# Kernel tuning notes

Hardware: AMD Instinct MI355X
Metric: run time of the kernel (lower is better)

The kernel has to match this reference:

```python
import jax, jax.numpy as jnp
import numpy as np

B, N, E, H, NE = 8, 512, 512, 8, 16384
DH = E // H
SCALE = DH ** -0.5
EPS = 1e-5


def _layernorm(x, g, b):
    mu = jnp.mean(x, axis=-1, keepdims=True)
    var = jnp.var(x, axis=-1, keepdims=True)
    return (x - mu) / jnp.sqrt(var + EPS) * g + b


def setup_inputs() -> dict:
    key = jax.random.key(0)
    ks = jax.random.split(key, 24)
    s = 0.02
    return {
        "x": jax.random.normal(ks[0], (B, N, E), jnp.float32),
        "edge_attr": jax.random.normal(ks[1], (NE, E), jnp.float32),
        "Wq": jax.random.normal(ks[2], (E, E), jnp.float32) * s,
        "bq": jnp.zeros((E,), jnp.float32),
        "Wk": jax.random.normal(ks[3], (E, E), jnp.float32) * s,
        "bk": jnp.zeros((E,), jnp.float32),
        "Wv": jax.random.normal(ks[4], (E, E), jnp.float32) * s,
        "bv": jnp.zeros((E,), jnp.float32),
        "Wo": jax.random.normal(ks[5], (E, E), jnp.float32) * s,
        "bo": jnp.zeros((E,), jnp.float32),
        "dist_table": jax.random.normal(ks[6], (100, H), jnp.float32),
        "We": jax.random.normal(ks[7], (H, E), jnp.float32) * s,
        "be": jnp.zeros((H,), jnp.float32),
        "W1": jax.random.normal(ks[8], (4 * E, E), jnp.float32) * s,
        "b1": jnp.zeros((4 * E,), jnp.float32),
        "W2": jax.random.normal(ks[9], (E, 4 * E), jnp.float32) * s,
        "b2": jnp.zeros((E,), jnp.float32),
        "g1": jnp.ones((E,), jnp.float32),
        "beta1": jnp.zeros((E,), jnp.float32),
        "g2": jnp.ones((E,), jnp.float32),
        "beta2": jnp.zeros((E,), jnp.float32),
        "edge_index": jax.random.randint(ks[10], (2, NE), 0, N, jnp.int64),
        "distance_matrix": jax.random.randint(ks[11], (B, N, N), 0, 100, jnp.int32),
    }


def reference(x, edge_attr, Wq, bq, Wk, bk, Wv, bv, Wo, bo, dist_table, We, be,
              W1, b1, W2, b2, g1, beta1, g2, beta2, edge_index, distance_matrix):
    residual = x
    h = _layernorm(x, g1, beta1)
    # projections -> [B, H, N, DH]
    def proj(W, b):
        return (h @ W.T + b).reshape(B, N, H, DH).transpose(0, 2, 1, 3)
    q, k, v = proj(Wq, bq), proj(Wk, bk), proj(Wv, bv)
    attn = jnp.einsum('bhnd,bhmd->bhnm', q, k) * SCALE
    # distance-encoding gather: [B,N,N] -> [B,N,N,H] -> [B,H,N,N]
    d_idx = jnp.clip(distance_matrix, 0, 99)
    attn = attn + dist_table[d_idx].transpose(0, 3, 1, 2)
    # per-edge scatter-add bias (duplicates accumulate, matching sequential loop)
    edge_enc = (edge_attr @ We.T + be).T  # [H, NE]
    src, tgt = edge_index[0], edge_index[1]
    edge_bias = jnp.zeros((H, N, N), attn.dtype).at[:, src, tgt].add(edge_enc)
    attn = attn + edge_bias[None]
    attn = jax.nn.softmax(attn, axis=-1)
    out = jnp.einsum('bhnm,bhmd->bhnd', attn, v)
    out = out.transpose(0, 2, 1, 3).reshape(B, N, E)
    out = out @ Wo.T + bo
    x1 = residual + out
    h2 = _layernorm(x1, g2, beta2)
    ffn = jax.nn.gelu(h2 @ W1.T + b1, approximate=False) @ W2.T + b2
    return x1 + ffn
```

## Files before the change

kernel.cpp:

```cpp
#include <hip/hip_runtime.h>
#include <cstdint>
#include <cstddef>

#define B_  8
#define N_  512
#define E_  512
#define H_  8
#define DH_ 64
#define NE_ 16384
#define QT  64

using u16   = unsigned short;
using bf16x8 = __attribute__((ext_vector_type(8))) __bf16;
using u16x8  = __attribute__((ext_vector_type(8))) unsigned short;
using f32x4  = __attribute__((ext_vector_type(4))) float;

__device__ __forceinline__ u16 f2b(float f) {
  unsigned u = __builtin_bit_cast(unsigned, f);
  u += 0x7fffu + ((u >> 16) & 1u);
  return (u16)(u >> 16);
}

__device__ __forceinline__ bf16x8 ld_frag(const u16* p) {
  return __builtin_bit_cast(bf16x8, *(const u16x8*)p);
}

__device__ __forceinline__ void gld_lds16(const u16* g, u16* l) {
  __builtin_amdgcn_global_load_lds(
      (const __attribute__((address_space(1))) unsigned*)(g),
      (__attribute__((address_space(3))) unsigned*)(l), 16, 0, 0);
}

__device__ __forceinline__ void gemm_core_128x128(
    const u16* __restrict__ At, int lda,
    const u16* __restrict__ Bt, int ldb, int K,
    u16* ldsA, u16* ldsB, f32x4 (&acc)[4][4]) {
  const int tid  = threadIdx.x;
  const int wid  = tid >> 6, lane = tid & 63;
  const int wr   = wid >> 1, wc = wid & 1;
  const int qd   = lane >> 4, r = lane & 15;
  const int mrow = tid >> 2, k0 = (tid & 3) * 8;
  const int wbase = wid << 9;
  for (int kt = 0; kt < K; kt += 32) {
    __syncthreads();
    gld_lds16(&At[(size_t)mrow*lda + kt + k0],        ldsA + wbase);
    gld_lds16(&At[(size_t)(mrow+64)*lda + kt + k0],   ldsA + 64*32 + wbase);
    gld_lds16(&Bt[(size_t)mrow*ldb + kt + k0],        ldsB + wbase);
    gld_lds16(&Bt[(size_t)(mrow+64)*ldb + kt + k0],   ldsB + 64*32 + wbase);
    __syncthreads();
    bf16x8 af[4], bfv[4];
#pragma unroll
    for (int i = 0; i < 4; ++i) af[i] = ld_frag(&ldsA[(wr*64 + i*16 + r)*32 + qd*8]);
#pragma unroll
    for (int j = 0; j < 4; ++j) bfv[j] = ld_frag(&ldsB[(wc*64 + j*16 + r)*32 + qd*8]);
#pragma unroll
    for (int i = 0; i < 4; ++i)
#pragma unroll
      for (int j = 0; j < 4; ++j)
        acc[i][j] = __builtin_amdgcn_mfma_f32_16x16x32_bf16(af[i], bfv[j], acc[i][j], 0, 0, 0);
  }
}

template <int EPI>
__global__ __launch_bounds__(256) void gemm_epi(
    const u16* __restrict__ A, const u16* __restrict__ W,
    const float* __restrict__ bias, const float* __restrict__ res,
    float* __restrict__ outf, u16* __restrict__ outb, int Kd, int Nd) {
  __shared__ u16 ldsA[128*32];
  __shared__ u16 ldsB[128*32];
  const int bx = blockIdx.x, by = blockIdx.y;
  f32x4 acc[4][4] = {};
  gemm_core_128x128(A + (size_t)bx*128*Kd, Kd, W + (size_t)by*128*Kd, Kd, Kd,
                    ldsA, ldsB, acc);
  const int tid = threadIdx.x, wid = tid>>6, lane = tid&63;
  const int wr = wid>>1, wc = wid&1, qd = lane>>4, r = lane&15;
#pragma unroll
  for (int i = 0; i < 4; ++i) {
#pragma unroll
    for (int j = 0; j < 4; ++j) {
      const int grow = bx*128 + wr*64 + i*16 + qd*4;
      const int gcol = by*128 + wc*64 + j*16 + r;
      const float bb = bias[gcol];
#pragma unroll
      for (int rg = 0; rg < 4; ++rg) {
        float v = acc[i][j][rg] + bb;
        const size_t idx = (size_t)(grow + rg)*Nd + gcol;
        if constexpr (EPI == 0) {
          outb[idx] = f2b(v);
        } else if constexpr (EPI == 1) {
          outf[idx] = v + res[idx];
        } else {
          v = 0.5f * v * (1.0f + erff(v * 0.70710678118f));
          outb[idx] = f2b(v);
        }
      }
    }
  }
}

__global__ __launch_bounds__(256) void gemm_splitk_k(
    const u16* __restrict__ A, const u16* __restrict__ W,
    float* __restrict__ part, int Kd, int Nd, int Ks) {
  __shared__ u16 ldsA[128*32];
  __shared__ u16 ldsB[128*32];
  const int bx = blockIdx.x, by = blockIdx.y, s = blockIdx.z;
  f32x4 acc[4][4] = {};
  gemm_core_128x128(A + (size_t)bx*128*Kd + (size_t)s*Ks, Kd,
                    W + (size_t)by*128*Kd + (size_t)s*Ks, Kd, Ks,
                    ldsA, ldsB, acc);
  const int tid = threadIdx.x, wid = tid>>6, lane = tid&63;
  const int wr = wid>>1, wc = wid&1, qd = lane>>4, r = lane&15;
  float* po = part + (size_t)s*(B_*N_)*Nd;
#pragma unroll
  for (int i = 0; i < 4; ++i) {
#pragma unroll
    for (int j = 0; j < 4; ++j) {
      const int grow = bx*128 + wr*64 + i*16 + qd*4;
      const int gcol = by*128 + wc*64 + j*16 + r;
#pragma unroll
      for (int rg = 0; rg < 4; ++rg)
        po[(size_t)(grow + rg)*Nd + gcol] = acc[i][j][rg];
    }
  }
}

template <int S>
__global__ __launch_bounds__(256) void splitk_reduce_k(
    const float* __restrict__ part, const float* __restrict__ bias,
    const float* __restrict__ res, float* __restrict__ out) {
  const size_t base = ((size_t)blockIdx.x*256 + threadIdx.x) * 4;
  float4 v = *(const float4*)&res[base];
  const int col = (int)(base & (E_-1));
  const float4 bb = *(const float4*)&bias[col];
  v.x += bb.x; v.y += bb.y; v.z += bb.z; v.w += bb.w;
#pragma unroll
  for (int s = 0; s < S; ++s) {
    const float4 p = *(const float4*)&part[(size_t)s*(B_*N_*E_) + base];
    v.x += p.x; v.y += p.y; v.z += p.z; v.w += p.w;
  }
  *(float4*)&out[base] = v;
}

__device__ __forceinline__ void ln_store(
    float v0, float v1, const float* __restrict__ g,
    const float* __restrict__ be, u16* __restrict__ outb, int row, int t) {
  float s = v0 + v1, ss = v0*v0 + v1*v1;
  for (int o = 32; o; o >>= 1) { s += __shfl_down(s, o); ss += __shfl_down(ss, o); }
  __shared__ float rs[4], rss[4];
  const int wid = t>>6, lane = t&63;
  if (!lane) { rs[wid] = s; rss[wid] = ss; }
  __syncthreads();
  s  = rs[0]+rs[1]+rs[2]+rs[3];
  ss = rss[0]+rss[1]+rss[2]+rss[3];
  const float mu   = s * (1.0f/E_);
  const float var  = ss * (1.0f/E_) - mu*mu;
  const float rstd = rsqrtf(var + 1e-5f);
  outb[(size_t)row*E_ + t]       = f2b((v0-mu)*rstd*g[t] + be[t]);
  outb[(size_t)row*E_ + t + 256] = f2b((v1-mu)*rstd*g[t+256] + be[t+256]);
}

__global__ __launch_bounds__(256) void splitk_reduce_ln_k(
    const float* __restrict__ part, const float* __restrict__ bias,
    const float* __restrict__ res, float* __restrict__ x1,
    const float* __restrict__ g, const float* __restrict__ be,
    u16* __restrict__ h2b) {
  const int row = blockIdx.x, t = threadIdx.x;
  const size_t base = (size_t)row*E_;
  float v0 = res[base + t]       + bias[t];
  float v1 = res[base + t + 256] + bias[t + 256];
#pragma unroll
  for (int s = 0; s < 2; ++s) {
    v0 += part[(size_t)s*(B_*N_*E_) + base + t];
    v1 += part[(size_t)s*(B_*N_*E_) + base + t + 256];
  }
  x1[base + t] = v0; x1[base + t + 256] = v1;
  ln_store(v0, v1, g, be, h2b, row, t);
}

__global__ __launch_bounds__(256) void qkv_gemm_k(
    const u16* __restrict__ A,
    const u16* __restrict__ Wqb, const u16* __restrict__ Wkb, const u16* __restrict__ Wvb,
    const float* __restrict__ bq, const float* __restrict__ bk, const float* __restrict__ bv,
    u16* __restrict__ qo, u16* __restrict__ ko, u16* __restrict__ vo) {
  __shared__ u16 ldsA[128*32];
  __shared__ u16 ldsB[128*32];
  const int bx = blockIdx.x, by = blockIdx.y, z = blockIdx.z;
  const u16*   W    = z == 0 ? Wqb : (z == 1 ? Wkb : Wvb);
  const float* bias = z == 0 ? bq  : (z == 1 ? bk  : bv);
  u16*         outb = z == 0 ? qo  : (z == 1 ? ko  : vo);
  f32x4 acc[4][4] = {};
  gemm_core_128x128(A + (size_t)bx*128*E_, E_, W + (size_t)by*128*E_, E_, E_,
                    ldsA, ldsB, acc);
  const int tid = threadIdx.x, wid = tid>>6, lane = tid&63;
  const int wr = wid>>1, wc = wid&1, qd = lane>>4, r = lane&15;
#pragma unroll
  for (int i = 0; i < 4; ++i) {
#pragma unroll
    for (int j = 0; j < 4; ++j) {
      const int grow = bx*128 + wr*64 + i*16 + qd*4;
      const int gcol = by*128 + wc*64 + j*16 + r;
      const float bb = bias[gcol];
#pragma unroll
      for (int rg = 0; rg < 4; ++rg)
        outb[(size_t)(grow + rg)*E_ + gcol] = f2b(acc[i][j][rg] + bb);
    }
  }
}

__global__ __launch_bounds__(256) void flash_attn_k(
    const u16* __restrict__ qm, const u16* __restrict__ km, const u16* __restrict__ vm,
    const float* __restrict__ dtab, const int* __restrict__ Dm,
    const float* __restrict__ ebias, u16* __restrict__ outb) {
  __shared__ u16 sK[2*128*32];
  __shared__ u16 sP[64*136];
  __shared__ u16 sVt[64*136];
  __shared__ float sDt[104];
  __shared__ float sMax[2][QT], sSum[2][QT], sM[QT], sL[QT], sAlpha[QT];

  const int bx = blockIdx.x;
  const int bz = blockIdx.y; const int b = bz>>3, h = bz&7;
  const int n0 = bx*QT;
  const int tid = threadIdx.x, wid = tid>>6, lane = tid&63;
  const int wr = wid>>1, wc = wid&1, qd = lane>>4, r = lane&15;
  const int lrow = lane>>2, lk = (lane&3)*8;

  const u16* Qg = qm + ((size_t)(b*N_ + n0))*E_ + h*DH_;
  const u16* Kg = km + (size_t)b*N_*E_ + h*DH_;
  const u16* Vg = vm + (size_t)b*N_*E_ + h*DH_;
  const int*   Db = Dm + (size_t)b*N_*N_;
  const float* Eb = ebias + (size_t)h*N_*N_;

#pragma unroll
  for (int ks = 0; ks < 2; ++ks)
    gld_lds16(&Qg[(size_t)(wid*16 + lrow)*E_ + ks*32 + lk], sP + ks*2048 + wid*512);
  for (int idx = tid; idx < 100; idx += 256) sDt[idx] = dtab[idx*H_ + h];
  if (tid < QT) { sM[tid] = -3.0e38f; sL[tid] = 0.f; }
  __syncthreads();
  bf16x8 qf[2][2];
#pragma unroll
  for (int ks = 0; ks < 2; ++ks)
#pragma unroll
    for (int i = 0; i < 2; ++i)
      qf[ks][i] = ld_frag(&sP[ks*2048 + (wr*32 + i*16 + r)*32 + qd*8]);

  f32x4 accO[2][2] = {};

  for (int mc = 0; mc < N_; mc += 128) {
    __syncthreads();
#pragma unroll
    for (int t = 0; t < 2; ++t) {
      const int row0 = wid*32 + t*16;
#pragma unroll
      for (int ks = 0; ks < 2; ++ks)
        gld_lds16(&Kg[(size_t)(mc + row0 + lrow)*E_ + ks*32 + lk],
                  sK + ks*4096 + row0*32);
    }
#pragma unroll
    for (int it = 0; it < 4; ++it) {
      const int idx = it*256 + tid;
      const int m = idx>>3, d0 = (idx&7)*8;
      const int g = d0>>3;
      const u16x8 u = *(const u16x8*)&Vg[(size_t)(mc+m)*E_ + d0];
      const int msw = m ^ (0 );
#pragma unroll
      for (int e = 0; e < 8; ++e) {
        sVt[(d0+e)*136 + (m ^ (g<<3))] = u[e];
      }
      (void)msw;
    }
    __syncthreads();
    f32x4 accS[2][4] = {};
#pragma unroll
    for (int ks = 0; ks < 2; ++ks) {
      bf16x8 bfv[4];
#pragma unroll
      for (int j = 0; j < 4; ++j)
        bfv[j] = ld_frag(&sK[ks*4096 + (wc*64 + j*16 + r)*32 + qd*8]);
#pragma unroll
      for (int i = 0; i < 2; ++i)
#pragma unroll
        for (int j = 0; j < 4; ++j)
          accS[i][j] = __builtin_amdgcn_mfma_f32_16x16x32_bf16(qf[ks][i], bfv[j], accS[i][j], 0, 0, 0);
    }
    float rmax[2][4];
#pragma unroll
    for (int i = 0; i < 2; ++i)
#pragma unroll
      for (int rg = 0; rg < 4; ++rg) rmax[i][rg] = -3.0e38f;
#pragma unroll
    for (int i = 0; i < 2; ++i) {
      const int n = n0 + wr*32 + i*16 + qd*4;
#pragma unroll
      for (int j = 0; j < 4; ++j) {
        const int m = mc + wc*64 + j*16 + r;
#pragma unroll
        for (int rg = 0; rg < 4; ++rg) {
          int di = Db[(size_t)(n+rg)*N_ + m];
          di = di < 0 ? 0 : (di > 99 ? 99 : di);
          const float v = accS[i][j][rg]*0.125f + sDt[di] + Eb[(size_t)(n+rg)*N_ + m];
          accS[i][j][rg] = v;
          rmax[i][rg] = fmaxf(rmax[i][rg], v);
        }
      }
    }
#pragma unroll
    for (int i = 0; i < 2; ++i)
#pragma unroll
      for (int rg = 0; rg < 4; ++rg) {
        float v = rmax[i][rg];
        v = fmaxf(v, __shfl_xor(v, 1)); v = fmaxf(v, __shfl_xor(v, 2));
        v = fmaxf(v, __shfl_xor(v, 4)); v = fmaxf(v, __shfl_xor(v, 8));
        if (r == 0) sMax[wc][wr*32 + i*16 + qd*4 + rg] = v;
      }
    __syncthreads();
    if (tid < QT) {
      const float mcx  = fmaxf(sMax[0][tid], sMax[1][tid]);
      const float mnew = fmaxf(sM[tid], mcx);
      sAlpha[tid] = __expf(sM[tid] - mnew);
      sM[tid] = mnew;
    }
    __syncthreads();
    float rsum[2][4];
#pragma unroll
    for (int i = 0; i < 2; ++i) {
      const int lr0 = wr*32 + i*16 + qd*4;
#pragma unroll
      for (int rg = 0; rg < 4; ++rg) {
        const float mrow = sM[lr0 + rg];
        float partial = 0.f;
#pragma unroll
        for (int j = 0; j < 4; ++j) {
          const float p = __expf(accS[i][j][rg] - mrow);
          partial += p;
          sP[(lr0+rg)*136 + wc*64 + j*16 + r] = f2b(p);
        }
        rsum[i][rg] = partial;
        const float a = sAlpha[lr0 + rg];
#pragma unroll
        for (int jj = 0; jj < 2; ++jj) accO[i][jj][rg] *= a;
      }
    }
#pragma unroll
    for (int i = 0; i < 2; ++i)
#pragma unroll
      for (int rg = 0; rg < 4; ++rg) {
        float v = rsum[i][rg];
        v += __shfl_xor(v, 1); v += __shfl_xor(v, 2);
        v += __shfl_xor(v, 4); v += __shfl_xor(v, 8);
        if (r == 0) sSum[wc][wr*32 + i*16 + qd*4 + rg] = v;
      }
    __syncthreads();
    if (tid < QT) sL[tid] = sL[tid]*sAlpha[tid] + sSum[0][tid] + sSum[1][tid];
    __syncthreads();
#pragma unroll
    for (int ks = 0; ks < 4; ++ks) {
      bf16x8 af[2], bfv[2];
#pragma unroll
      for (int i = 0; i < 2; ++i)
        af[i] = ld_frag(&sP[(wr*32 + i*16 + r)*136 + ks*32 + qd*8]);
#pragma unroll
      for (int jj = 0; jj < 2; ++jj) {
        const int d = wc*32 + jj*16 + r;
        const int mb = (ks*32 + qd*8) ^ (((d>>3)&7)<<3);
        bfv[jj] = ld_frag(&sVt[d*136 + mb]);
      }
#pragma unroll
      for (int i = 0; i < 2; ++i)
#pragma unroll
        for (int jj = 0; jj < 2; ++jj)
          accO[i][jj] = __builtin_amdgcn_mfma_f32_16x16x32_bf16(af[i], bfv[jj], accO[i][jj], 0, 0, 0);
    }
  }
#pragma unroll
  for (int i = 0; i < 2; ++i) {
    const int lr0 = wr*32 + i*16 + qd*4;
#pragma unroll
    for (int jj = 0; jj < 2; ++jj) {
      const int d = wc*32 + jj*16 + r;
#pragma unroll
      for (int rg = 0; rg < 4; ++rg) {
        const float inv = 1.0f / sL[lr0 + rg];
        outb[((size_t)(b*N_ + n0 + lr0 + rg))*E_ + h*DH_ + d] = f2b(accO[i][jj][rg] * inv);
      }
    }
  }
}

#define SEG0 32768
#define SEG1 65536
#define SEG2 98304
#define SEG3 131072
#define SEG4 262144
#define SEG5 393216
__global__ __launch_bounds__(256) void prep_k(
    const float* __restrict__ Wq, const float* __restrict__ Wk,
    const float* __restrict__ Wv, const float* __restrict__ Wo,
    const float* __restrict__ W1, const float* __restrict__ W2,
    u16* __restrict__ wq_b, u16* __restrict__ wk_b, u16* __restrict__ wv_b,
    u16* __restrict__ wo_b, u16* __restrict__ w1_b, u16* __restrict__ w2_b,
    const float* __restrict__ x, const float* __restrict__ g1,
    const float* __restrict__ bet1, u16* __restrict__ h_b) {
  if (blockIdx.x < 1536) {
    const int i = blockIdx.x*256 + threadIdx.x;
    const float* src; u16* dst; int base;
    if      (i < SEG0) { src = Wq; dst = wq_b; base = 0; }
    else if (i < SEG1) { src = Wk; dst = wk_b; base = SEG0; }
    else if (i < SEG2) { src = Wv; dst = wv_b; base = SEG1; }
    else if (i < SEG3) { src = Wo; dst = wo_b; base = SEG2; }
    else if (i < SEG4) { src = W1; dst = w1_b; base = SEG3; }
    else               { src = W2; dst = w2_b; base = SEG4; }
    const int li = i - base;
    const float4 f0 = *(const float4*)&src[(size_t)li*8];
    const float4 f1 = *(const float4*)&src[(size_t)li*8 + 4];
    u16x8 u;
    u[0]=f2b(f0.x); u[1]=f2b(f0.y); u[2]=f2b(f0.z); u[3]=f2b(f0.w);
    u[4]=f2b(f1.x); u[5]=f2b(f1.y); u[6]=f2b(f1.z); u[7]=f2b(f1.w);
    *(u16x8*)&dst[(size_t)li*8] = u;
  } else {
    const int row = blockIdx.x - 1536, t = threadIdx.x;
    const float v0 = x[(size_t)row*E_ + t], v1 = x[(size_t)row*E_ + t + 256];
    ln_store(v0, v1, g1, bet1, h_b, row, t);
  }
}

__global__ __launch_bounds__(256) void edge_enc_scatter_k(
    const float* __restrict__ ea, const float* __restrict__ We,
    const float* __restrict__ be, const int* __restrict__ ei,
    float* __restrict__ eb) {
  const int wglob = (blockIdx.x*256 + threadIdx.x) >> 6;
  const int lane  = threadIdx.x & 63;
  float w[8][8];
#pragma unroll
  for (int h = 0; h < 8; ++h) {
    const float4 f0 = *(const float4*)&We[h*E_ + lane*8];
    const float4 f1 = *(const float4*)&We[h*E_ + lane*8 + 4];
    w[h][0]=f0.x; w[h][1]=f0.y; w[h][2]=f0.z; w[h][3]=f0.w;
    w[h][4]=f1.x; w[h][5]=f1.y; w[h][6]=f1.z; w[h][7]=f1.w;
  }
  const float beh = (lane < 8) ? be[lane] : 0.f;
#pragma unroll 1
  for (int t = 0; t < NE_/2048; ++t) {
    const int e = wglob*(NE_/2048) + t;
    const float* ar = ea + (size_t)e*E_;
    const float4 a0 = *(const float4*)&ar[lane*8];
    const float4 a1 = *(const float4*)&ar[lane*8 + 4];
    const float a[8] = {a0.x,a0.y,a0.z,a0.w,a1.x,a1.y,a1.z,a1.w};
    float acc[8];
#pragma unroll
    for (int h = 0; h < 8; ++h) {
      float s = 0.f;
#pragma unroll
      for (int j = 0; j < 8; ++j) s += a[j]*w[h][j];
      acc[h] = s;
    }
#pragma unroll
    for (int h = 0; h < 8; ++h) {
      float v = acc[h];
      v += __shfl_xor(v, 1);  v += __shfl_xor(v, 2);  v += __shfl_xor(v, 4);
      v += __shfl_xor(v, 8);  v += __shfl_xor(v, 16); v += __shfl_xor(v, 32);
      acc[h] = v;
    }
    float myv = acc[0];
#pragma unroll
    for (int h = 1; h < 8; ++h) myv = (lane == h) ? acc[h] : myv;
    if (lane < 8) {
      const int s2 = ei[e], t2 = ei[NE_ + e];
      atomicAdd(&eb[((size_t)lane*N_ + s2)*N_ + t2], myv + beh);
    }
  }
}

extern "C" void kernel_launch(void* const* d_in, const int* in_sizes, int n_in,
                              void* d_out, int out_size, void* d_ws, size_t ws_size,
                              hipStream_t stream) {
  const float* x     = (const float*)d_in[0];
  const float* ea    = (const float*)d_in[1];
  const float* Wq    = (const float*)d_in[2];
  const float* bq    = (const float*)d_in[3];
  const float* Wk    = (const float*)d_in[4];
  const float* bk    = (const float*)d_in[5];
  const float* Wv    = (const float*)d_in[6];
  const float* bv    = (const float*)d_in[7];
  const float* Wo    = (const float*)d_in[8];
  const float* bo    = (const float*)d_in[9];
  const float* dtab  = (const float*)d_in[10];
  const float* We    = (const float*)d_in[11];
  const float* be    = (const float*)d_in[12];
  const float* W1    = (const float*)d_in[13];
  const float* b1    = (const float*)d_in[14];
  const float* W2    = (const float*)d_in[15];
  const float* b2    = (const float*)d_in[16];
  const float* g1    = (const float*)d_in[17];
  const float* bet1  = (const float*)d_in[18];
  const float* g2    = (const float*)d_in[19];
  const float* bet2  = (const float*)d_in[20];
  const int*   eidx  = (const int*)d_in[21];
  const int*   Dmat  = (const int*)d_in[22];
  float* out = (float*)d_out;

  char* ws = (char*)d_ws;
  size_t off = 0;
  auto alloc = [&](size_t bytes) -> void* {
    void* p = ws + off;
    off += (bytes + 255) & ~(size_t)255;
    return p;
  };
  u16* wq_b = (u16*)alloc((size_t)E_*E_*2);
  u16* wk_b = (u16*)alloc((size_t)E_*E_*2);
  u16* wv_b = (u16*)alloc((size_t)E_*E_*2);
  u16* wo_b = (u16*)alloc((size_t)E_*E_*2);
  u16* w1_b = (u16*)alloc((size_t)4*E_*E_*2);
  u16* w2_b = (u16*)alloc((size_t)4*E_*E_*2);
  u16* h_b  = (u16*)alloc((size_t)B_*N_*E_*2);
  u16* q_b  = (u16*)alloc((size_t)B_*N_*E_*2);
  u16* k_b  = (u16*)alloc((size_t)B_*N_*E_*2);
  u16* v_b  = (u16*)alloc((size_t)B_*N_*E_*2);
  float* ebias = (float*)alloc((size_t)H_*N_*N_*4);
  float* x1    = (float*)alloc((size_t)B_*N_*E_*4);
  u16*   h2_b  = (u16*)alloc((size_t)B_*N_*E_*2);
  u16*   mid_b = (u16*)alloc((size_t)B_*N_*4*E_*2);
  float* part  = (float*)alloc((size_t)4*B_*N_*E_*4);
  u16*   ao_b  = h_b;

  const int M = B_*N_;

  prep_k<<<dim3(1536 + M), 256, 0, stream>>>(
      Wq, Wk, Wv, Wo, W1, W2, wq_b, wk_b, wv_b, wo_b, w1_b, w2_b,
      x, g1, bet1, h_b);

  qkv_gemm_k<<<dim3(M/128, E_/128, 3), 256, 0, stream>>>(
      h_b, wq_b, wk_b, wv_b, bq, bk, bv, q_b, k_b, v_b);

  hipMemsetAsync(ebias, 0, (size_t)H_*N_*N_*4, stream);
  edge_enc_scatter_k<<<dim3(512), 256, 0, stream>>>(ea, We, be, eidx, ebias);

  flash_attn_k<<<dim3(N_/QT, B_*H_), 256, 0, stream>>>(
      q_b, k_b, v_b, dtab, Dmat, ebias, ao_b);

  gemm_splitk_k<<<dim3(M/128, E_/128, 2), 256, 0, stream>>>(
      ao_b, wo_b, part, E_, E_, E_/2);
  splitk_reduce_ln_k<<<dim3(M), 256, 0, stream>>>(
      part, bo, x, x1, g2, bet2, h2_b);

  gemm_epi<2><<<dim3(M/128, 4*E_/128), 256, 0, stream>>>(h2_b, w1_b, b1, nullptr, nullptr, mid_b, E_, 4*E_);

  gemm_splitk_k<<<dim3(M/128, E_/128, 4), 256, 0, stream>>>(
      mid_b, w2_b, part, 4*E_, E_, E_);
  splitk_reduce_k<4><<<dim3(M*E_/1024), 256, 0, stream>>>(part, b2, x1, out);
}
```

Baseline: 268.0 us.

## Fuse edge scatter into QKV launch, fold memset into prep, per-warp flash softmax

New measurement: 304.1 us. 13.5% more time.

```diff
diff --git a/kernel.cpp b/kernel.cpp
--- a/kernel.cpp
+++ b/kernel.cpp
@@ -177,14 +177,61 @@
   ln_store(v0, v1, g, be, h2b, row, t);
 }
 
-__global__ __launch_bounds__(256) void qkv_gemm_k(
+__global__ __launch_bounds__(256) void qkv_edge_k(
     const u16* __restrict__ A,
     const u16* __restrict__ Wqb, const u16* __restrict__ Wkb, const u16* __restrict__ Wvb,
     const float* __restrict__ bq, const float* __restrict__ bk, const float* __restrict__ bv,
-    u16* __restrict__ qo, u16* __restrict__ ko, u16* __restrict__ vo) {
+    u16* __restrict__ qo, u16* __restrict__ ko, u16* __restrict__ vo,
+    const float* __restrict__ ea, const float* __restrict__ We,
+    const float* __restrict__ be, const int* __restrict__ ei,
+    float* __restrict__ eb) {
   __shared__ u16 ldsA[128*32];
   __shared__ u16 ldsB[128*32];
   const int bx = blockIdx.x, by = blockIdx.y, z = blockIdx.z;
+  if (z == 3) {
+    const int wglob = ((by*32 + bx)*256 + (int)threadIdx.x) >> 6;
+    const int lane  = threadIdx.x & 63;
+    float w[8][8];
+#pragma unroll
+    for (int h = 0; h < 8; ++h) {
+      const float4 f0 = *(const float4*)&We[h*E_ + lane*8];
+      const float4 f1 = *(const float4*)&We[h*E_ + lane*8 + 4];
+      w[h][0]=f0.x; w[h][1]=f0.y; w[h][2]=f0.z; w[h][3]=f0.w;
+      w[h][4]=f1.x; w[h][5]=f1.y; w[h][6]=f1.z; w[h][7]=f1.w;
+    }
+    const float beh = (lane < 8) ? be[lane] : 0.f;
+#pragma unroll 1
+    for (int t = 0; t < NE_/512; ++t) {
+      const int e = wglob*(NE_/512) + t;
+      const float* ar = ea + (size_t)e*E_;
+      const float4 a0 = *(const float4*)&ar[lane*8];
+      const float4 a1 = *(const float4*)&ar[lane*8 + 4];
+      const float a[8] = {a0.x,a0.y,a0.z,a0.w,a1.x,a1.y,a1.z,a1.w};
+      float acc[8];
+#pragma unroll
+      for (int h = 0; h < 8; ++h) {
+        float s = 0.f;
+#pragma unroll
+        for (int j = 0; j < 8; ++j) s += a[j]*w[h][j];
+        acc[h] = s;
+      }
+#pragma unroll
+      for (int h = 0; h < 8; ++h) {
+        float v = acc[h];
+        v += __shfl_xor(v, 1);  v += __shfl_xor(v, 2);  v += __shfl_xor(v, 4);
+        v += __shfl_xor(v, 8);  v += __shfl_xor(v, 16); v += __shfl_xor(v, 32);
+        acc[h] = v;
+      }
+      float myv = acc[0];
+#pragma unroll
+      for (int h = 1; h < 8; ++h) myv = (lane == h) ? acc[h] : myv;
+      if (lane < 8) {
+        const int s2 = ei[e], t2 = ei[NE_ + e];
+        atomicAdd(&eb[((size_t)lane*N_ + s2)*N_ + t2], myv + beh);
+      }
+    }
+    return;
+  }
   const u16*   W    = z == 0 ? Wqb : (z == 1 ? Wkb : Wvb);
   const float* bias = z == 0 ? bq  : (z == 1 ? bk  : bv);
   u16*         outb = z == 0 ? qo  : (z == 1 ? ko  : vo);
@@ -212,38 +259,34 @@
     const float* __restrict__ dtab, const int* __restrict__ Dm,
     const float* __restrict__ ebias, u16* __restrict__ outb) {
   __shared__ u16 sK[2*128*32];
-  __shared__ u16 sP[64*136];
   __shared__ u16 sVt[64*136];
+  __shared__ u16 sP[4*16*136];
   __shared__ float sDt[104];
-  __shared__ float sMax[2][QT], sSum[2][QT], sM[QT], sL[QT], sAlpha[QT];
 
   const int bx = blockIdx.x;
   const int bz = blockIdx.y; const int b = bz>>3, h = bz&7;
   const int n0 = bx*QT;
   const int tid = threadIdx.x, wid = tid>>6, lane = tid&63;
-  const int wr = wid>>1, wc = wid&1, qd = lane>>4, r = lane&15;
+  const int qd = lane>>4, r = lane&15;
   const int lrow = lane>>2, lk = (lane&3)*8;
 
-  const u16* Qg = qm + ((size_t)(b*N_ + n0))*E_ + h*DH_;
+  const u16* Qg = qm + ((size_t)(b*N_ + n0 + wid*16))*E_ + h*DH_;
   const u16* Kg = km + (size_t)b*N_*E_ + h*DH_;
   const u16* Vg = vm + (size_t)b*N_*E_ + h*DH_;
   const int*   Db = Dm + (size_t)b*N_*N_;
   const float* Eb = ebias + (size_t)h*N_*N_;
-
+  u16* sPw = sP + wid*16*136;
+
+  bf16x8 qf[2];
 #pragma unroll
   for (int ks = 0; ks < 2; ++ks)
-    gld_lds16(&Qg[(size_t)(wid*16 + lrow)*E_ + ks*32 + lk], sP + ks*2048 + wid*512);
+    qf[ks] = ld_frag(&Qg[(size_t)r*E_ + ks*32 + qd*8]);
   for (int idx = tid; idx < 100; idx += 256) sDt[idx] = dtab[idx*H_ + h];
-  if (tid < QT) { sM[tid] = -3.0e38f; sL[tid] = 0.f; }
-  __syncthreads();
-  bf16x8 qf[2][2];
-#pragma unroll
-  for (int ks = 0; ks < 2; ++ks)
-#pragma unroll
-    for (int i = 0; i < 2; ++i)
-      qf[ks][i] = ld_frag(&sP[ks*2048 + (wr*32 + i*16 + r)*32 + qd*8]);
-
-  f32x4 accO[2][2] = {};
+
+  float mI[4], lI[4];
+#pragma unroll
+  for (int rg = 0; rg < 4; ++rg) { mI[rg] = -3.0e38f; lI[rg] = 0.f; }
+  f32x4 accO[4] = {};
 
   for (int mc = 0; mc < N_; mc += 128) {
     __syncthreads();
@@ -261,127 +304,81 @@
       const int m = idx>>3, d0 = (idx&7)*8;
       const int g = d0>>3;
       const u16x8 u = *(const u16x8*)&Vg[(size_t)(mc+m)*E_ + d0];
-      const int msw = m ^ (0 );
-#pragma unroll
-      for (int e = 0; e < 8; ++e) {
+#pragma unroll
+      for (int e = 0; e < 8; ++e)
         sVt[(d0+e)*136 + (m ^ (g<<3))] = u[e];
-      }
-      (void)msw;
     }
     __syncthreads();
-    f32x4 accS[2][4] = {};
-#pragma unroll
-    for (int ks = 0; ks < 2; ++ks) {
-      bf16x8 bfv[4];
-#pragma unroll
-      for (int j = 0; j < 4; ++j)
-        bfv[j] = ld_frag(&sK[ks*4096 + (wc*64 + j*16 + r)*32 + qd*8]);
-#pragma unroll
-      for (int i = 0; i < 2; ++i)
-#pragma unroll
-        for (int j = 0; j < 4; ++j)
-          accS[i][j] = __builtin_amdgcn_mfma_f32_16x16x32_bf16(qf[ks][i], bfv[j], accS[i][j], 0, 0, 0);
-    }
-    float rmax[2][4];
-#pragma unroll
-    for (int i = 0; i < 2; ++i)
-#pragma unroll
-      for (int rg = 0; rg < 4; ++rg) rmax[i][rg] = -3.0e38f;
-#pragma unroll
-    for (int i = 0; i < 2; ++i) {
-      const int n = n0 + wr*32 + i*16 + qd*4;
-#pragma unroll
-      for (int j = 0; j < 4; ++j) {
-        const int m = mc + wc*64 + j*16 + r;
-#pragma unroll
-        for (int rg = 0; rg < 4; ++rg) {
-          int di = Db[(size_t)(n+rg)*N_ + m];
-          di = di < 0 ? 0 : (di > 99 ? 99 : di);
-          const float v = accS[i][j][rg]*0.125f + sDt[di] + Eb[(size_t)(n+rg)*N_ + m];
-          accS[i][j][rg] = v;
-          rmax[i][rg] = fmaxf(rmax[i][rg], v);
-        }
-      }
-    }
-#pragma unroll
-    for (int i = 0; i < 2; ++i)
+    f32x4 accS[8] = {};
+#pragma unroll
+    for (int ks = 0; ks < 2; ++ks)
+#pragma unroll
+      for (int j = 0; j < 8; ++j) {
+        const bf16x8 bfv = ld_frag(&sK[ks*4096 + (j*16 + r)*32 + qd*8]);
+        accS[j] = __builtin_amdgcn_mfma_f32_16x16x32_bf16(qf[ks], bfv, accS[j], 0, 0, 0);
+      }
+    float nmax[4];
+#pragma unroll
+    for (int rg = 0; rg < 4; ++rg) nmax[rg] = -3.0e38f;
+    const int nbase = n0 + wid*16 + qd*4;
+#pragma unroll
+    for (int j = 0; j < 8; ++j) {
+      const int m = mc + j*16 + r;
 #pragma unroll
       for (int rg = 0; rg < 4; ++rg) {
-        float v = rmax[i][rg];
-        v = fmaxf(v, __shfl_xor(v, 1)); v = fmaxf(v, __shfl_xor(v, 2));
-        v = fmaxf(v, __shfl_xor(v, 4)); v = fmaxf(v, __shfl_xor(v, 8));
-        if (r == 0) sMax[wc][wr*32 + i*16 + qd*4 + rg] = v;
-      }
-    __syncthreads();
-    if (tid < QT) {
-      const float mcx  = fmaxf(sMax[0][tid], sMax[1][tid]);
-      const float mnew = fmaxf(sM[tid], mcx);
-      sAlpha[tid] = __expf(sM[tid] - mnew);
-      sM[tid] = mnew;
-    }
-    __syncthreads();
-    float rsum[2][4];
-#pragma unroll
-    for (int i = 0; i < 2; ++i) {
-      const int lr0 = wr*32 + i*16 + qd*4;
-#pragma unroll
-      for (int rg = 0; rg < 4; ++rg) {
-        const float mrow = sM[lr0 + rg];
-        float partial = 0.f;
-#pragma unroll
-        for (int j = 0; j < 4; ++j) {
-          const float p = __expf(accS[i][j][rg] - mrow);
-          partial += p;
-          sP[(lr0+rg)*136 + wc*64 + j*16 + r] = f2b(p);
-        }
-        rsum[i][rg] = partial;
-        const float a = sAlpha[lr0 + rg];
-#pragma unroll
-        for (int jj = 0; jj < 2; ++jj) accO[i][jj][rg] *= a;
-      }
-    }
-#pragma unroll
-    for (int i = 0; i < 2; ++i)
-#pragma unroll
-      for (int rg = 0; rg < 4; ++rg) {
-        float v = rsum[i][rg];
-        v += __shfl_xor(v, 1); v += __shfl_xor(v, 2);
-        v += __shfl_xor(v, 4); v += __shfl_xor(v, 8);
-        if (r == 0) sSum[wc][wr*32 + i*16 + qd*4 + rg] = v;
-      }
-    __syncthreads();
-    if (tid < QT) sL[tid] = sL[tid]*sAlpha[tid] + sSum[0][tid] + sSum[1][tid];
-    __syncthreads();
-#pragma unroll
-    for (int ks = 0; ks < 4; ++ks) {
-      bf16x8 af[2], bfv[2];
-#pragma unroll
-      for (int i = 0; i < 2; ++i)
-        af[i] = ld_frag(&sP[(wr*32 + i*16 + r)*136 + ks*32 + qd*8]);
-#pragma unroll
-      for (int jj = 0; jj < 2; ++jj) {
-        const int d = wc*32 + jj*16 + r;
-        const int mb = (ks*32 + qd*8) ^ (((d>>3)&7)<<3);
-        bfv[jj] = ld_frag(&sVt[d*136 + mb]);
-      }
-#pragma unroll
-      for (int i = 0; i < 2; ++i)
-#pragma unroll
-        for (int jj = 0; jj < 2; ++jj)
-          accO[i][jj] = __builtin_amdgcn_mfma_f32_16x16x32_bf16(af[i], bfv[jj], accO[i][jj], 0, 0, 0);
-    }
-  }
-#pragma unroll
-  for (int i = 0; i < 2; ++i) {
-    const int lr0 = wr*32 + i*16 + qd*4;
-#pragma unroll
-    for (int jj = 0; jj < 2; ++jj) {
-      const int d = wc*32 + jj*16 + r;
-#pragma unroll
-      for (int rg = 0; rg < 4; ++rg) {
-        const float inv = 1.0f / sL[lr0 + rg];
-        outb[((size_t)(b*N_ + n0 + lr0 + rg))*E_ + h*DH_ + d] = f2b(accO[i][jj][rg] * inv);
-      }
+        int di = Db[(size_t)(nbase+rg)*N_ + m];
+        di = di < 0 ? 0 : (di > 99 ? 99 : di);
+        const float v = accS[j][rg]*0.125f + sDt[di] + Eb[(size_t)(nbase+rg)*N_ + m];
+        accS[j][rg] = v;
+        nmax[rg] = fmaxf(nmax[rg], v);
+      }
+    }
+    float alph[4];
+#pragma unroll
+    for (int rg = 0; rg < 4; ++rg) {
+      float v = nmax[rg];
+      v = fmaxf(v, __shfl_xor(v, 1)); v = fmaxf(v, __shfl_xor(v, 2));
+      v = fmaxf(v, __shfl_xor(v, 4)); v = fmaxf(v, __shfl_xor(v, 8));
+      const float mnew = fmaxf(mI[rg], v);
+      alph[rg] = __expf(mI[rg] - mnew);
+      mI[rg] = mnew;
+    }
+#pragma unroll
+    for (int rg = 0; rg < 4; ++rg) {
+      const float mrow = mI[rg];
+      float partial = 0.f;
+#pragma unroll
+      for (int j = 0; j < 8; ++j) {
+        const float p = __expf(accS[j][rg] - mrow);
+        partial += p;
+        sPw[(qd*4+rg)*136 + j*16 + r] = f2b(p);
+      }
+      float v = partial;
+      v += __shfl_xor(v, 1); v += __shfl_xor(v, 2);
+      v += __shfl_xor(v, 4); v += __shfl_xor(v, 8);
+      lI[rg] = lI[rg]*alph[rg] + v;
+#pragma unroll
+      for (int t = 0; t < 4; ++t) accO[t][rg] *= alph[rg];
+    }
+#pragma unroll
+    for (int ks2 = 0; ks2 < 4; ++ks2) {
+      const bf16x8 af = ld_frag(&sPw[r*136 + ks2*32 + qd*8]);
+#pragma unroll
+      for (int t = 0; t < 4; ++t) {
+        const int d = t*16 + r;
+        const int mb = (ks2*32 + qd*8) ^ (((d>>3)&7)<<3);
+        const bf16x8 bfv = ld_frag(&sVt[d*136 + mb]);
+        accO[t] = __builtin_amdgcn_mfma_f32_16x16x32_bf16(af, bfv, accO[t], 0, 0, 0);
+      }
+    }
+  }
+#pragma unroll
+  for (int t = 0; t < 4; ++t) {
+    const int d = t*16 + r;
+#pragma unroll
+    for (int rg = 0; rg < 4; ++rg) {
+      const int row = n0 + wid*16 + qd*4 + rg;
+      outb[((size_t)(b*N_ + row))*E_ + h*DH_ + d] = f2b(accO[t][rg] / lI[rg]);
     }
   }
 }
@@ -392,6 +389,9 @@
 #define SEG3 131072
 #define SEG4 262144
 #define SEG5 393216
+#define PREP_LN0   1536
+#define PREP_EB0   (1536 + 4096)
+#define PREP_NB    (PREP_EB0 + 2048)
 __global__ __launch_bounds__(256) void prep_k(
     const float* __restrict__ Wq, const float* __restrict__ Wk,
     const float* __restrict__ Wv, const float* __restrict__ Wo,
@@ -399,8 +399,9 @@
     u16* __restrict__ wq_b, u16* __restrict__ wk_b, u16* __restrict__ wv_b,
     u16* __restrict__ wo_b, u16* __restrict__ w1_b, u16* __restrict__ w2_b,
     const float* __restrict__ x, const float* __restrict__ g1,
-    const float* __restrict__ bet1, u16* __restrict__ h_b) {
-  if (blockIdx.x < 1536) {
+    const float* __restrict__ bet1, u16* __restrict__ h_b,
+    float* __restrict__ ebias) {
+  if (blockIdx.x < PREP_LN0) {
     const int i = blockIdx.x*256 + threadIdx.x;
     const float* src; u16* dst; int base;
     if      (i < SEG0) { src = Wq; dst = wq_b; base = 0; }
@@ -416,57 +417,13 @@
     u[0]=f2b(f0.x); u[1]=f2b(f0.y); u[2]=f2b(f0.z); u[3]=f2b(f0.w);
     u[4]=f2b(f1.x); u[5]=f2b(f1.y); u[6]=f2b(f1.z); u[7]=f2b(f1.w);
     *(u16x8*)&dst[(size_t)li*8] = u;
-  } else {
-    const int row = blockIdx.x - 1536, t = threadIdx.x;
+  } else if (blockIdx.x < PREP_EB0) {
+    const int row = blockIdx.x - PREP_LN0, t = threadIdx.x;
     const float v0 = x[(size_t)row*E_ + t], v1 = x[(size_t)row*E_ + t + 256];
     ln_store(v0, v1, g1, bet1, h_b, row, t);
-  }
-}
-
-__global__ __launch_bounds__(256) void edge_enc_scatter_k(
-    const float* __restrict__ ea, const float* __restrict__ We,
-    const float* __restrict__ be, const int* __restrict__ ei,
-    float* __restrict__ eb) {
-  const int wglob = (blockIdx.x*256 + threadIdx.x) >> 6;
-  const int lane  = threadIdx.x & 63;
-  float w[8][8];
-#pragma unroll
-  for (int h = 0; h < 8; ++h) {
-    const float4 f0 = *(const float4*)&We[h*E_ + lane*8];
-    const float4 f1 = *(const float4*)&We[h*E_ + lane*8 + 4];
-    w[h][0]=f0.x; w[h][1]=f0.y; w[h][2]=f0.z; w[h][3]=f0.w;
-    w[h][4]=f1.x; w[h][5]=f1.y; w[h][6]=f1.z; w[h][7]=f1.w;
-  }
-  const float beh = (lane < 8) ? be[lane] : 0.f;
-#pragma unroll 1
-  for (int t = 0; t < NE_/2048; ++t) {
-    const int e = wglob*(NE_/2048) + t;
-    const float* ar = ea + (size_t)e*E_;
-    const float4 a0 = *(const float4*)&ar[lane*8];
-    const float4 a1 = *(const float4*)&ar[lane*8 + 4];
-    const float a[8] = {a0.x,a0.y,a0.z,a0.w,a1.x,a1.y,a1.z,a1.w};
-    float acc[8];
-#pragma unroll
-    for (int h = 0; h < 8; ++h) {
-      float s = 0.f;
-#pragma unroll
-      for (int j = 0; j < 8; ++j) s += a[j]*w[h][j];
-      acc[h] = s;
-    }
-#pragma unroll
-    for (int h = 0; h < 8; ++h) {
-      float v = acc[h];
-      v += __shfl_xor(v, 1);  v += __shfl_xor(v, 2);  v += __shfl_xor(v, 4);
-      v += __shfl_xor(v, 8);  v += __shfl_xor(v, 16); v += __shfl_xor(v, 32);
-      acc[h] = v;
-    }
-    float myv = acc[0];
-#pragma unroll
-    for (int h = 1; h < 8; ++h) myv = (lane == h) ? acc[h] : myv;
-    if (lane < 8) {
-      const int s2 = ei[e], t2 = ei[NE_ + e];
-      atomicAdd(&eb[((size_t)lane*N_ + s2)*N_ + t2], myv + beh);
-    }
+  } else {
+    const size_t i = ((size_t)(blockIdx.x - PREP_EB0)*256 + threadIdx.x)*4;
+    *(float4*)&ebias[i] = float4{0.f, 0.f, 0.f, 0.f};
   }
 }
 
@@ -524,15 +481,13 @@
 
   const int M = B_*N_;
 
-  prep_k<<<dim3(1536 + M), 256, 0, stream>>>(
+  prep_k<<<dim3(PREP_NB), 256, 0, stream>>>(
       Wq, Wk, Wv, Wo, W1, W2, wq_b, wk_b, wv_b, wo_b, w1_b, w2_b,
-      x, g1, bet1, h_b);
-
-  qkv_gemm_k<<<dim3(M/128, E_/128, 3), 256, 0, stream>>>(
-      h_b, wq_b, wk_b, wv_b, bq, bk, bv, q_b, k_b, v_b);
-
-  hipMemsetAsync(ebias, 0, (size_t)H_*N_*N_*4, stream);
-  edge_enc_scatter_k<<<dim3(512), 256, 0, stream>>>(ea, We, be, eidx, ebias);
+      x, g1, bet1, h_b, ebias);
+
+  qkv_edge_k<<<dim3(M/128, E_/128, 4), 256, 0, stream>>>(
+      h_b, wq_b, wk_b, wv_b, bq, bk, bv, q_b, k_b, v_b,
+      ea, We, be, eidx, ebias);
 
   flash_attn_k<<<dim3(N_/QT, B_*H_), 256, 0, stream>>>(
       q_b, k_b, v_b, dtab, Dmat, ebias, ao_b);
```

## Split attention over key halves with combine kernel; fold ebias zeroing into prep

Applied to the files above, without the earlier changes.

Result: slower. 276.8 us (+3.3%).

```diff
diff --git a/kernel.cpp b/kernel.cpp
--- a/kernel.cpp
+++ b/kernel.cpp
@@ -13,6 +13,7 @@
 using u16   = unsigned short;
 using bf16x8 = __attribute__((ext_vector_type(8))) __bf16;
 using u16x8  = __attribute__((ext_vector_type(8))) unsigned short;
+using u16x4  = __attribute__((ext_vector_type(4))) unsigned short;
 using f32x4  = __attribute__((ext_vector_type(4))) float;
 
 __device__ __forceinline__ u16 f2b(float f) {
@@ -210,7 +211,8 @@
 __global__ __launch_bounds__(256) void flash_attn_k(
     const u16* __restrict__ qm, const u16* __restrict__ km, const u16* __restrict__ vm,
     const float* __restrict__ dtab, const int* __restrict__ Dm,
-    const float* __restrict__ ebias, u16* __restrict__ outb) {
+    const float* __restrict__ ebias, float* __restrict__ Opart,
+    float* __restrict__ Mb, float* __restrict__ Lb) {
   __shared__ u16 sK[2*128*32];
   __shared__ u16 sP[64*136];
   __shared__ u16 sVt[64*136];
@@ -219,6 +221,7 @@
 
   const int bx = blockIdx.x;
   const int bz = blockIdx.y; const int b = bz>>3, h = bz&7;
+  const int mh = blockIdx.z;
   const int n0 = bx*QT;
   const int tid = threadIdx.x, wid = tid>>6, lane = tid&63;
   const int wr = wid>>1, wc = wid&1, qd = lane>>4, r = lane&15;
@@ -244,8 +247,9 @@
       qf[ks][i] = ld_frag(&sP[ks*2048 + (wr*32 + i*16 + r)*32 + qd*8]);
 
   f32x4 accO[2][2] = {};
-
-  for (int mc = 0; mc < N_; mc += 128) {
+  const int mbeg = mh*256;
+
+  for (int mc = mbeg; mc < mbeg + 256; mc += 128) {
     __syncthreads();
 #pragma unroll
     for (int t = 0; t < 2; ++t) {
@@ -261,12 +265,9 @@
       const int m = idx>>3, d0 = (idx&7)*8;
       const int g = d0>>3;
       const u16x8 u = *(const u16x8*)&Vg[(size_t)(mc+m)*E_ + d0];
-      const int msw = m ^ (0 );
-#pragma unroll
-      for (int e = 0; e < 8; ++e) {
+#pragma unroll
+      for (int e = 0; e < 8; ++e)
         sVt[(d0+e)*136 + (m ^ (g<<3))] = u[e];
-      }
-      (void)msw;
     }
     __syncthreads();
     f32x4 accS[2][4] = {};
@@ -371,6 +372,7 @@
           accO[i][jj] = __builtin_amdgcn_mfma_f32_16x16x32_bf16(af[i], bfv[jj], accO[i][jj], 0, 0, 0);
     }
   }
+  float* op = Opart + (size_t)mh*(B_*N_*E_);
 #pragma unroll
   for (int i = 0; i < 2; ++i) {
     const int lr0 = wr*32 + i*16 + qd*4;
@@ -378,12 +380,39 @@
     for (int jj = 0; jj < 2; ++jj) {
       const int d = wc*32 + jj*16 + r;
 #pragma unroll
-      for (int rg = 0; rg < 4; ++rg) {
-        const float inv = 1.0f / sL[lr0 + rg];
-        outb[((size_t)(b*N_ + n0 + lr0 + rg))*E_ + h*DH_ + d] = f2b(accO[i][jj][rg] * inv);
-      }
-    }
-  }
+      for (int rg = 0; rg < 4; ++rg)
+        op[((size_t)(b*N_ + n0 + lr0 + rg))*E_ + h*DH_ + d] = accO[i][jj][rg];
+    }
+  }
+  if (tid < QT) {
+    const size_t ml = ((size_t)mh*(B_*H_) + bz)*N_ + n0 + tid;
+    Mb[ml] = sM[tid];
+    Lb[ml] = sL[tid];
+  }
+}
+
+__global__ __launch_bounds__(256) void splitkv_combine_k(
+    const float* __restrict__ Opart, const float* __restrict__ Mb,
+    const float* __restrict__ Lb, u16* __restrict__ outb) {
+  const size_t base = ((size_t)blockIdx.x*256 + threadIdx.x) * 4;
+  const int nrow = (int)(base >> 9);
+  const int col  = (int)(base & 511);
+  const int b = nrow >> 9, n = nrow & 511;
+  const int h = col >> 6;
+  const size_t ml = ((size_t)(b*H_ + h))*N_ + n;
+  const float m0 = Mb[ml], l0 = Lb[ml];
+  const float m1 = Mb[(size_t)(B_*H_)*N_ + ml], l1 = Lb[(size_t)(B_*H_)*N_ + ml];
+  const float M = fmaxf(m0, m1);
+  const float a0 = __expf(m0 - M), a1 = __expf(m1 - M);
+  const float inv = 1.0f / (a0*l0 + a1*l1);
+  const float4 o0 = *(const float4*)&Opart[base];
+  const float4 o1 = *(const float4*)&Opart[(size_t)(B_*N_*E_) + base];
+  u16x4 o;
+  o[0] = f2b((a0*o0.x + a1*o1.x)*inv);
+  o[1] = f2b((a0*o0.y + a1*o1.y)*inv);
+  o[2] = f2b((a0*o0.z + a1*o1.z)*inv);
+  o[3] = f2b((a0*o0.w + a1*o1.w)*inv);
+  *(u16x4*)&outb[base] = o;
 }
 
 #define SEG0 32768
@@ -392,6 +421,9 @@
 #define SEG3 131072
 #define SEG4 262144
 #define SEG5 393216
+#define PREP_LN0   1536
+#define PREP_EB0   (1536 + 4096)
+#define PREP_NB    (PREP_EB0 + 2048)
 __global__ __launch_bounds__(256) void prep_k(
     const float* __restrict__ Wq, const float* __restrict__ Wk,
     const float* __restrict__ Wv, const float* __restrict__ Wo,
@@ -399,8 +431,9 @@
     u16* __restrict__ wq_b, u16* __restrict__ wk_b, u16* __restrict__ wv_b,
     u16* __restrict__ wo_b, u16* __restrict__ w1_b, u16* __restrict__ w2_b,
     const float* __restrict__ x, const float* __restrict__ g1,
-    const float* __restrict__ bet1, u16* __restrict__ h_b) {
-  if (blockIdx.x < 1536) {
+    const float* __restrict__ bet1, u16* __restrict__ h_b,
+    float* __restrict__ ebias) {
+  if (blockIdx.x < PREP_LN0) {
     const int i = blockIdx.x*256 + threadIdx.x;
     const float* src; u16* dst; int base;
     if      (i < SEG0) { src = Wq; dst = wq_b; base = 0; }
@@ -416,10 +449,13 @@
     u[0]=f2b(f0.x); u[1]=f2b(f0.y); u[2]=f2b(f0.z); u[3]=f2b(f0.w);
     u[4]=f2b(f1.x); u[5]=f2b(f1.y); u[6]=f2b(f1.z); u[7]=f2b(f1.w);
     *(u16x8*)&dst[(size_t)li*8] = u;
-  } else {
-    const int row = blockIdx.x - 1536, t = threadIdx.x;
+  } else if (blockIdx.x < PREP_EB0) {
+    const int row = blockIdx.x - PREP_LN0, t = threadIdx.x;
     const float v0 = x[(size_t)row*E_ + t], v1 = x[(size_t)row*E_ + t + 256];
     ln_store(v0, v1, g1, bet1, h_b, row, t);
+  } else {
+    const size_t i = ((size_t)(blockIdx.x - PREP_EB0)*256 + threadIdx.x)*4;
+    *(float4*)&ebias[i] = float4{0.f, 0.f, 0.f, 0.f};
   }
 }
 
@@ -520,22 +556,24 @@
   u16*   h2_b  = (u16*)alloc((size_t)B_*N_*E_*2);
   u16*   mid_b = (u16*)alloc((size_t)B_*N_*4*E_*2);
   float* part  = (float*)alloc((size_t)4*B_*N_*E_*4);
+  float* Mb    = (float*)alloc((size_t)2*B_*H_*N_*4);
+  float* Lb    = (float*)alloc((size_t)2*B_*H_*N_*4);
   u16*   ao_b  = h_b;
 
   const int M = B_*N_;
 
-  prep_k<<<dim3(1536 + M), 256, 0, stream>>>(
+  prep_k<<<dim3(PREP_NB), 256, 0, stream>>>(
       Wq, Wk, Wv, Wo, W1, W2, wq_b, wk_b, wv_b, wo_b, w1_b, w2_b,
-      x, g1, bet1, h_b);
+      x, g1, bet1, h_b, ebias);
 
   qkv_gemm_k<<<dim3(M/128, E_/128, 3), 256, 0, stream>>>(
       h_b, wq_b, wk_b, wv_b, bq, bk, bv, q_b, k_b, v_b);
 
-  hipMemsetAsync(ebias, 0, (size_t)H_*N_*N_*4, stream);
   edge_enc_scatter_k<<<dim3(512), 256, 0, stream>>>(ea, We, be, eidx, ebias);
 
-  flash_attn_k<<<dim3(N_/QT, B_*H_), 256, 0, stream>>>(
-      q_b, k_b, v_b, dtab, Dmat, ebias, ao_b);
+  flash_attn_k<<<dim3(N_/QT, B_*H_, 2), 256, 0, stream>>>(
+      q_b, k_b, v_b, dtab, Dmat, ebias, part, Mb, Lb);
+  splitkv_combine_k<<<dim3(M*E_/1024), 256, 0, stream>>>(part, Mb, Lb, ao_b);
 
   gemm_splitk_k<<<dim3(M/128, E_/128, 2), 256, 0, stream>>>(
       ao_b, wo_b, part, E_, E_, E_/2);
```
